# Kernel optimization log

Hardware: AMD Instinct MI355X
Metric: run time of the kernel (lower is better)

## Reference

```python
import jax, jax.numpy as jnp
import numpy as np

B, S, D, E = 2, 2048, 1024, 8
H = 2 * D          # hidden_dim = 2*n_embd
A = H // 16        # adapt_dim


def _ln(x, g, b):
    m = x.mean(-1, keepdims=True)
    v = x.var(-1, keepdims=True)
    return (x - m) * jax.lax.rsqrt(v + 1e-5) * g + b


def setup_inputs() -> dict:
    key = jax.random.key(0)
    ks = jax.random.split(key, 16)
    s = 1.0 / np.sqrt(D)        # shared-linear init scale
    sa = s * 0.01               # adapter-linear init scale
    sg = 0.01 / np.sqrt(A)      # expert adapter init scale
    f32 = jnp.float32
    return {
        "x": jax.random.normal(ks[0], (B, S, D), f32),
        "expert_weights": jax.nn.softmax(jax.random.normal(ks[1], (B * S, E), f32), -1),
        "up_w": jax.random.normal(ks[2], (H, D), f32) * s,
        "gate_w": jax.random.normal(ks[3], (H, D), f32) * s,
        "down_w": jax.random.normal(ks[4], (D, H), f32) * s,
        "pre_w": jax.random.normal(ks[5], (A, D), f32) * sa,
        "post_w": jax.random.normal(ks[6], (A, H), f32) * sa,
        "an_g": jnp.ones((A,), f32),
        "an_b": jnp.zeros((A,), f32),
        "adapt_proj_w": jax.random.normal(ks[7], (H, A), f32) * sa,
        "adapter_w": jax.random.normal(ks[8], (E, A, A), f32) * sg,
        "adapter_g": jnp.ones((E, A), f32),
        "adapter_b": jnp.zeros((E, A), f32),
        "expert_proj_w": jax.random.normal(ks[9], (H, A), f32) * sg,
        "output_proj_w": jax.random.normal(ks[10], (D, H), f32) * sg,
    }


def reference(x, expert_weights, up_w, gate_w, down_w, pre_w, post_w, an_g, an_b,
              adapt_proj_w, adapter_w, adapter_g, adapter_b, expert_proj_w, output_proj_w):
    # ---- SharedExpertMLP ----
    up = x @ up_w.T                                  # [B,S,H]
    gate = x @ gate_w.T                              # [B,S,H]
    hidden = jax.nn.silu(gate) * up                  # SwiGLU
    adapt_in = _ln(x @ pre_w.T, an_g, an_b)          # [B,S,A]
    adapt_out = _ln(hidden @ post_w.T, an_g, an_b)   # [B,S,A]
    w = jnp.einsum('bsa,bta->bst', adapt_in, adapt_out)
    w = jax.nn.silu(jnp.clip(w, -5.0, 5.0))          # clamp+SiLU score
    # explicit fp32 bmm as in original autocast-disabled block
    adapt = jnp.einsum('bst,bta->bsa',
                       w.astype(jnp.float32),
                       adapt_in.astype(jnp.float32)).astype(x.dtype)
    hidden = hidden + 0.1 * (adapt @ adapt_proj_w.T)
    shared_out = hidden @ down_w.T                   # [B,S,D] (dropout is identity in eval)

    # ---- per-token expert mixing ----
    xf = x.reshape(-1, x.shape[-1])                  # [N,D], N=B*S
    a = _ln(xf @ pre_w.T, an_g, an_b)                # [N,A]
    h = jnp.einsum('na,eca->nec', a, adapter_w)      # per-expert low-rank adapt [N,E,A]
    h = _ln(h, adapter_g[None], adapter_b[None])
    mixed = jnp.einsum('ne,nea->na', expert_weights, h)   # combine experts [N,A]
    out = (mixed @ expert_proj_w.T) @ output_proj_w.T     # [N,D]
    return shared_out + out.reshape(x.shape)
```

## Files before the change

### kernel.cpp

```cpp
#include <hip/hip_runtime.h>
#include <hip/hip_bf16.h>
#include <math.h>

#define Bq 2
#define Sq 2048
#define Dq 1024
#define Eq 8
#define Hq 2048
#define Aq 128
#define Nq (Bq*Sq)

typedef __attribute__((ext_vector_type(4))) float f32x4;
typedef __attribute__((ext_vector_type(8))) short bfrag;

__device__ __forceinline__ float silu_f(float x) {
    return x / (1.0f + expf(-x));
}
__device__ __forceinline__ unsigned short f2bf(float x) {
    unsigned u = __float_as_uint(x);
    u += 0x7fffu + ((u >> 16) & 1u);
    return (unsigned short)(u >> 16);
}
__device__ __forceinline__ float bf2f(unsigned short h) {
    return __uint_as_float(((unsigned)h) << 16);
}
__device__ __forceinline__ void gl16(const unsigned short* g, unsigned short* l) {
    __builtin_amdgcn_global_load_lds(
        (const __attribute__((address_space(1))) void*)g,
        (__attribute__((address_space(3))) void*)(void*)l, 16, 0, 0);
}

#define WAITV_BAR(N)                                            \
    asm volatile("s_waitcnt vmcnt(" #N ")" ::: "memory");       \
    __builtin_amdgcn_s_barrier();                               \
    asm volatile("" ::: "memory")
#define END_BAR()                                               \
    asm volatile("" ::: "memory");                              \
    __builtin_amdgcn_s_barrier();                               \
    asm volatile("" ::: "memory")
#define WAITV(N) asm volatile("s_waitcnt vmcnt(" #N ")" ::: "memory")
#define BARF()                                                  \
    asm volatile("" ::: "memory");                              \
    __builtin_amdgcn_s_barrier();                               \
    asm volatile("" ::: "memory")

__global__ __launch_bounds__(256)
void convert_all(const float* __restrict__ x,  const float* __restrict__ gw,
                 const float* __restrict__ uw, const float* __restrict__ dw,
                 const float* __restrict__ pw, const float* __restrict__ ow,
                 const float* __restrict__ opw, const float* __restrict__ aw,
                 const float* __restrict__ apw, const float* __restrict__ epw,
                 unsigned short* xh,  unsigned short* gwh, unsigned short* uwh,
                 unsigned short* dwh, unsigned short* pwh, unsigned short* powh,
                 unsigned short* oph, unsigned short* adw, unsigned short* apT)
{
    __shared__ float t[32][33];
    if (blockIdx.x >= 2048) {
        int bid = blockIdx.x - 2048;
        int z   = bid >> 8;
        int rem = bid & 255;
        int bx  = rem & 3, by = rem >> 2;
        const float* in = z ? epw : apw;
        unsigned short* out = apT + (size_t)z * Hq * Aq;
        int tx = threadIdx.x & 31, ty = threadIdx.x >> 5;
        int r0 = by * 32, c0 = bx * 32;
#pragma unroll
        for (int j = 0; j < 4; j++)
            t[ty + j * 8][tx] = in[(size_t)(r0 + ty + j * 8) * Aq + c0 + tx];
        __syncthreads();
#pragma unroll
        for (int j = 0; j < 4; j++)
            out[(size_t)(c0 + ty + j * 8) * Hq + r0 + tx] = f2bf(t[tx][ty + j * 8]);
        return;
    }
    const int T = 3276800;
    for (int i = blockIdx.x * 256 + threadIdx.x; i < T; i += 2048 * 256) {
        const float* in; unsigned short* hi; int j = i;
        if (j < 1048576)                 { in = x;   hi = xh;  }
        else if ((j -= 1048576) < 524288){ in = gw;  hi = gwh; }
        else if ((j -= 524288) < 524288) { in = uw;  hi = uwh; }
        else if ((j -= 524288) < 524288) { in = dw;  hi = dwh; }
        else if ((j -= 524288) < 32768)  { in = pw;  hi = pwh; }
        else if ((j -= 32768) < 65536)   { in = ow;  hi = powh; }
        else if ((j -= 65536) < 524288)  { in = opw; hi = oph; }
        else { j -= 524288;                in = aw;  hi = adw; }
        float4 v = ((const float4*)in)[j];
        ((ushort4*)hi)[j] = make_ushort4(f2bf(v.x), f2bf(v.y), f2bf(v.z), f2bf(v.w));
    }
}

template<int EPI>
__global__ __launch_bounds__(512)
void mg(const unsigned short* __restrict__ Ah, const unsigned short* __restrict__ Bh,
        void* __restrict__ Cv, int N, int K, int kchunks,
        long zA, long zB, long zC, long pz)
{
    __shared__ __align__(16) unsigned short lds[32768];

    const int tid = threadIdx.x;
    const int l   = tid & 63;
    const int w   = tid >> 6;
    const int wr  = w >> 2, wc = w & 3;
    const int bm0 = blockIdx.y * 128, bn0 = blockIdx.x * 128;
    const int bz  = blockIdx.z / kchunks;
    const int kz  = blockIdx.z - bz * kchunks;
    const int kcnt = K / kchunks;
    const int kbeg = kz * kcnt;
    const int kend = kbeg + kcnt;

    const unsigned short* A0 = Ah + (size_t)bz * zA;
    const unsigned short* B0 = Bh + (size_t)bz * zB;

    const int srow = tid >> 3;
    const int sq   = (tid & 7) ^ (srow & 7);
    const size_t aoff = (size_t)(bm0 + srow) * K + sq * 8;
    const size_t boff = (size_t)(bn0 + srow) * K + sq * 8;
    const size_t r64  = (size_t)64 * K;

    auto stage = [&](int b, int kt) {
        unsigned short* d = &lds[b * 16384 + (w << 9)];
        gl16(A0 + aoff + kt,       d + 0);
        gl16(A0 + aoff + kt + r64, d + 4096);
        gl16(B0 + boff + kt,       d + 8192);
        gl16(B0 + boff + kt + r64, d + 12288);
    };

    const int rowa = (wr * 64 + (l & 15)) * 64;
    const int rowb = (wc * 32 + (l & 15)) * 64;
    const int q0 = (((l >> 4)    ) ^ (l & 7)) << 3;
    const int q1 = (((l >> 4) + 4) ^ (l & 7)) << 3;

    f32x4 acc[4][2];
#pragma unroll
    for (int i = 0; i < 4; i++)
#pragma unroll
        for (int j = 0; j < 2; j++) acc[i][j] = (f32x4){0.f, 0.f, 0.f, 0.f};

    stage(0, kbeg);
    int cur = 0;
    for (int kt = kbeg; kt < kend; kt += 64) {
        if (kt + 64 < kend) {
            stage(cur ^ 1, kt + 64);
            WAITV_BAR(4);
        } else {
            WAITV_BAR(0);
        }
        const int cb = cur * 16384;
#pragma unroll
        for (int ks = 0; ks < 2; ks++) {
            const int qo = ks ? q1 : q0;
            bfrag a4[4], b4[2];
#pragma unroll
            for (int f = 0; f < 4; f++)
                a4[f] = *(const bfrag*)&lds[cb + rowa + f * 1024 + qo];
#pragma unroll
            for (int f = 0; f < 2; f++)
                b4[f] = *(const bfrag*)&lds[cb + 8192 + rowb + f * 1024 + qo];
#pragma unroll
            for (int i = 0; i < 4; i++)
#pragma unroll
                for (int j = 0; j < 2; j++)
                    acc[i][j] = __builtin_amdgcn_mfma_f32_16x16x32_bf16(a4[i], b4[j], acc[i][j], 0, 0, 0);
        }
        END_BAR();
        cur ^= 1;
    }

    const int crow0 = bm0 + wr * 64 + (l >> 4) * 4;
    const int ccol0 = bn0 + wc * 32 + (l & 15);
#pragma unroll
    for (int i = 0; i < 4; i++)
#pragma unroll
        for (int j = 0; j < 2; j++)
#pragma unroll
            for (int r = 0; r < 4; r++) {
                size_t idx = (size_t)(crow0 + i * 16 + r) * N + (ccol0 + j * 16);
                float v = acc[i][j][r];
                if (EPI == 0)
                    ((float*)Cv + (size_t)bz * zC + (size_t)kz * pz)[idx] = v;
                else if (EPI == 1)
                    ((unsigned short*)Cv + (size_t)bz * zC)[idx] =
                        f2bf(silu_f(fminf(fmaxf(v, -5.f), 5.f)));
                else
                    ((unsigned short*)Cv + (size_t)bz * zC)[idx] = f2bf(v);
            }
}

__global__ __launch_bounds__(512)
void gsc(const unsigned short* __restrict__ ainh, const unsigned short* __restrict__ aouth,
         const unsigned short* __restrict__ ainT, float* __restrict__ p3)
{
    __shared__ __align__(16) unsigned short lds[65536];
    const int AIN = 0, AOUT = 16384, AINT = 32768, PB = 49152;

    const int tid = threadIdx.x;
    const int l   = tid & 63;
    const int w   = tid >> 6;
    const int wr  = w >> 2, wc = w & 3;
    const int tz  = blockIdx.x;
    const int ib  = blockIdx.y;
    const int b   = blockIdx.z;
    const long SA = (long)Sq * Aq;

    auto stage32 = [&](int base, const unsigned short* src, size_t kstride) {
#pragma unroll
        for (int rd = 0; rd < 4; rd++) {
            int grow = rd * 32 + (w << 2) + (l >> 4);
            int slot = (l & 15) ^ (grow & 15);
            gl16(src + (size_t)grow * kstride + slot * 8,
                 &lds[base + rd * 4096 + (w << 9)]);
        }
    };

    const unsigned short* ainI_src = ainh + (size_t)b * SA + (size_t)(ib * 128) * Aq;
    f32x4 acc2[4][2];
#pragma unroll
    for (int i = 0; i < 4; i++)
#pragma unroll
        for (int j = 0; j < 2; j++) acc2[i][j] = (f32x4){0.f, 0.f, 0.f, 0.f};

    {
        int tglob = tz * 2;
        stage32(AIN,  ainI_src, Aq);
        stage32(AOUT, aouth + (size_t)b * SA + (size_t)(tglob * 128) * Aq, Aq);
        stage32(AINT, ainT  + (size_t)b * SA + (size_t)(tglob * 128), Sq);
        WAITV_BAR(0);
    }

    const int rowa = (wr * 64 + (l & 15)) * 128;
    const int rowb = (wc * 32 + (l & 15)) * 128;

#pragma unroll 1
    for (int t = 0; t < 2; t++) {
        if (t == 1) {
            int tglob = tz * 2 + 1;
            stage32(AOUT, aouth + (size_t)b * SA + (size_t)(tglob * 128) * Aq, Aq);
            stage32(AINT, ainT  + (size_t)b * SA + (size_t)(tglob * 128), Sq);
            WAITV_BAR(0);
        }
        f32x4 acc1[4][2];
#pragma unroll
        for (int i = 0; i < 4; i++)
#pragma unroll
            for (int j = 0; j < 2; j++) acc1[i][j] = (f32x4){0.f, 0.f, 0.f, 0.f};
#pragma unroll
        for (int ks = 0; ks < 4; ks++) {
            const int qo = ((ks * 4 + (l >> 4)) ^ (l & 15)) << 3;
            bfrag a4[4], b4[2];
#pragma unroll
            for (int f = 0; f < 4; f++)
                a4[f] = *(const bfrag*)&lds[AIN + rowa + f * 2048 + qo];
#pragma unroll
            for (int f = 0; f < 2; f++)
                b4[f] = *(const bfrag*)&lds[AOUT + rowb + f * 2048 + qo];
#pragma unroll
            for (int i = 0; i < 4; i++)
#pragma unroll
                for (int j = 0; j < 2; j++)
                    acc1[i][j] = __builtin_amdgcn_mfma_f32_16x16x32_bf16(a4[i], b4[j], acc1[i][j], 0, 0, 0);
        }
        {
            const int prow0 = wr * 64 + (l >> 4) * 4;
            const int pcol0 = wc * 32 + (l & 15);
#pragma unroll
            for (int i = 0; i < 4; i++)
#pragma unroll
                for (int j = 0; j < 2; j++)
#pragma unroll
                    for (int r = 0; r < 4; r++) {
                        int pr = prow0 + i * 16 + r;
                        int pc = pcol0 + j * 16;
                        float v = silu_f(fminf(fmaxf(acc1[i][j][r], -5.f), 5.f));
                        lds[PB + pr * 128 + (((pc >> 3) ^ (pr & 15)) << 3) + (pc & 7)] = f2bf(v);
                    }
        }
        __syncthreads();
#pragma unroll
        for (int ks = 0; ks < 4; ks++) {
            const int qo = ((ks * 4 + (l >> 4)) ^ (l & 15)) << 3;
            bfrag a4[4], b4[2];
#pragma unroll
            for (int f = 0; f < 4; f++)
                a4[f] = *(const bfrag*)&lds[PB + rowa + f * 2048 + qo];
#pragma unroll
            for (int f = 0; f < 2; f++)
                b4[f] = *(const bfrag*)&lds[AINT + rowb + f * 2048 + qo];
#pragma unroll
            for (int i = 0; i < 4; i++)
#pragma unroll
                for (int j = 0; j < 2; j++)
                    acc2[i][j] = __builtin_amdgcn_mfma_f32_16x16x32_bf16(a4[i], b4[j], acc2[i][j], 0, 0, 0);
        }
        __syncthreads();
    }

    const int crow0 = wr * 64 + (l >> 4) * 4;
    const int ccol0 = wc * 32 + (l & 15);
    float* dst = p3 + ((size_t)(b * 8 + tz) * Sq + ib * 128) * Aq;
#pragma unroll
    for (int i = 0; i < 4; i++)
#pragma unroll
        for (int j = 0; j < 2; j++)
#pragma unroll
            for (int r = 0; r < 4; r++)
                dst[(size_t)(crow0 + i * 16 + r) * Aq + ccol0 + j * 16] = acc2[i][j][r];
}

__global__ __launch_bounds__(512)
void gup(const unsigned short* __restrict__ xh, const unsigned short* __restrict__ gwh,
         const unsigned short* __restrict__ uwh, unsigned short* __restrict__ hh)
{
    __shared__ __align__(16) unsigned short lds[65536];
    const int tid = threadIdx.x;
    const int l   = tid & 63;
    const int w   = tid >> 6;
    const int wr  = w >> 2;
    const int wc  = w & 3;

    int id  = blockIdx.y * gridDim.x + blockIdx.x;
    int xcd = id & 7, j0 = id >> 3;
    int bx  = (xcd & 3) * 4 + (j0 & 3);
    int by  = (xcd >> 2) * 8 + (j0 >> 2);
    const int bm0 = by * 256, bn0 = bx * 128;

    const int srw = tid >> 3;
    const int sq  = (tid & 7) ^ (srw & 7);
    auto stageU = [&](int b, int u, int kt) {
        unsigned short* d = &lds[b * 32768 + u * 8192 + (tid << 3)];
        const unsigned short* src = (u < 2) ? xh : (u == 2 ? gwh : uwh);
        int baserow = (u < 2) ? (bm0 + u * 128) : bn0;
        size_t o = (size_t)(baserow + srw) * Dq + kt + sq * 8;
        gl16(src + o,                   d);
        gl16(src + o + (size_t)64 * Dq, d + 4096);
    };

    const int rowa = (wr * 128 + (l & 15)) * 64;
    const int rowb = (wc * 32  + (l & 15)) * 64;
    const int q0 = (((l >> 4)    ) ^ (l & 7)) << 3;
    const int q1 = (((l >> 4) + 4) ^ (l & 7)) << 3;

    f32x4 accg[8][2], accu[8][2];
#pragma unroll
    for (int i = 0; i < 8; i++)
#pragma unroll
        for (int jj = 0; jj < 2; jj++) {
            accg[i][jj] = (f32x4){0.f, 0.f, 0.f, 0.f};
            accu[i][jj] = (f32x4){0.f, 0.f, 0.f, 0.f};
        }

    stageU(0, 0, 0); stageU(0, 1, 0); stageU(0, 2, 0); stageU(0, 3, 0);
    int cur = 0;
    for (int kt = 0; kt < Dq; kt += 64) {
        const int pf = (kt + 64 < Dq);
        const int cb = cur * 32768;
        const int nx = cur ^ 1;
        bfrag a4[8], b4[2];

        WAITV(2);
        BARF();
#pragma unroll
        for (int f = 0; f < 8; f++)
            a4[f] = *(const bfrag*)&lds[cb + rowa + f * 1024 + q0];
#pragma unroll
        for (int f = 0; f < 2; f++)
            b4[f] = *(const bfrag*)&lds[cb + 16384 + rowb + f * 1024 + q0];
        if (pf) stageU(nx, 0, kt + 64);
        __builtin_amdgcn_s_setprio(1);
#pragma unroll
        for (int i = 0; i < 8; i++)
#pragma unroll
            for (int jj = 0; jj < 2; jj++)
                accg[i][jj] = __builtin_amdgcn_mfma_f32_16x16x32_bf16(a4[i], b4[jj], accg[i][jj], 0, 0, 0);
        __builtin_amdgcn_s_setprio(0);

        if (pf) { WAITV(2); } else { WAITV(0); }
        BARF();
#pragma unroll
        for (int f = 0; f < 2; f++)
            b4[f] = *(const bfrag*)&lds[cb + 24576 + rowb + f * 1024 + q0];
        if (pf) stageU(nx, 1, kt + 64);
        __builtin_amdgcn_s_setprio(1);
#pragma unroll
        for (int i = 0; i < 8; i++)
#pragma unroll
            for (int jj = 0; jj < 2; jj++)
                accu[i][jj] = __builtin_amdgcn_mfma_f32_16x16x32_bf16(a4[i], b4[jj], accu[i][jj], 0, 0, 0);
        __builtin_amdgcn_s_setprio(0);

        BARF();
#pragma unroll
        for (int f = 0; f < 8; f++)
            a4[f] = *(const bfrag*)&lds[cb + rowa + f * 1024 + q1];
#pragma unroll
        for (int f = 0; f < 2; f++)
            b4[f] = *(const bfrag*)&lds[cb + 16384 + rowb + f * 1024 + q1];
        if (pf) stageU(nx, 2, kt + 64);
        __builtin_amdgcn_s_setprio(1);
#pragma unroll
        for (int i = 0; i < 8; i++)
#pragma unroll
            for (int jj = 0; jj < 2; jj++)
                accg[i][jj] = __builtin_amdgcn_mfma_f32_16x16x32_bf16(a4[i], b4[jj], accg[i][jj], 0, 0, 0);
        __builtin_amdgcn_s_setprio(0);

        BARF();
#pragma unroll
        for (int f = 0; f < 2; f++)
            b4[f] = *(const bfrag*)&lds[cb + 24576 + rowb + f * 1024 + q1];
        if (pf) stageU(nx, 3, kt + 64);
        __builtin_amdgcn_s_setprio(1);
#pragma unroll
        for (int i = 0; i < 8; i++)
#pragma unroll
            for (int jj = 0; jj < 2; jj++)
                accu[i][jj] = __builtin_amdgcn_mfma_f32_16x16x32_bf16(a4[i], b4[jj], accu[i][jj], 0, 0, 0);
        __builtin_amdgcn_s_setprio(0);

        cur = nx;
    }

    const int crow0 = bm0 + wr * 128 + (l >> 4) * 4;
    const int ccol0 = bn0 + wc * 32 + (l & 15);
#pragma unroll
    for (int i = 0; i < 8; i++)
#pragma unroll
        for (int jj = 0; jj < 2; jj++)
#pragma unroll
            for (int r = 0; r < 4; r++) {
                size_t idx = (size_t)(crow0 + i * 16 + r) * Hq + (ccol0 + jj * 16);
                hh[idx] = f2bf(silu_f(accg[i][jj][r]) * accu[i][jj][r]);
            }
}

__global__ __launch_bounds__(512)
void gfinal(const unsigned short* __restrict__ hh, const unsigned short* __restrict__ dwh,
            const unsigned short* __restrict__ acat, const unsigned short* __restrict__ kcat,
            float* __restrict__ out)
{
    __shared__ __align__(16) unsigned short lds[49152];
    const int tid = threadIdx.x;
    const int l   = tid & 63;
    const int w   = tid >> 6;
    const int wr  = w >> 2, wc = w & 3;

    int nb  = gridDim.x * gridDim.y;
    int id  = blockIdx.y * gridDim.x + blockIdx.x;
    int id2 = (id & 7) * (nb >> 3) + (id >> 3);
    int bx  = id2 % gridDim.x, by = id2 / gridDim.x;
    const int bm0 = by * 128, bn0 = bx * 128;

    const int srow = tid >> 3;
    const int sq   = (tid & 7) ^ (srow & 7);
    const int rowa = (wr * 64 + (l & 15)) * 64;
    const int rowb = (wc * 32 + (l & 15)) * 64;
    const int q0 = (((l >> 4)    ) ^ (l & 7)) << 3;
    const int q1 = (((l >> 4) + 4) ^ (l & 7)) << 3;

    f32x4 acc[4][2];
#pragma unroll
    for (int i = 0; i < 4; i++)
#pragma unroll
        for (int j = 0; j < 2; j++) acc[i][j] = (f32x4){0.f, 0.f, 0.f, 0.f};

    {
        const size_t aoff = (size_t)(bm0 + srow) * Hq + sq * 8;
        const size_t boff = (size_t)(bn0 + srow) * Hq + sq * 8;
        const size_t r64  = (size_t)64 * Hq;
        auto stage = [&](int b, int kt) {
            unsigned short* d = &lds[b * 16384 + (w << 9)];
            gl16(hh  + aoff + kt,       d + 0);
            gl16(hh  + aoff + kt + r64, d + 4096);
            gl16(dwh + boff + kt,       d + 8192);
            gl16(dwh + boff + kt + r64, d + 12288);
        };
        stage(0, 0);
        stage(1, 64);
        int cur = 0;
        for (int kt = 0; kt < Hq; kt += 64) {
            if (kt + 64 < Hq) { WAITV_BAR(4); } else { WAITV_BAR(0); }
            if (kt + 128 < Hq) {
                int nb3 = (cur + 2 >= 3) ? cur - 1 : cur + 2;
                stage(nb3, kt + 128);
            }
            const int cb = cur * 16384;
#pragma unroll
            for (int ks = 0; ks < 2; ks++) {
                const int qo = ks ? q1 : q0;
                bfrag a4[4], b4[2];
#pragma unroll
                for (int f = 0; f < 4; f++)
                    a4[f] = *(const bfrag*)&lds[cb + rowa + f * 1024 + qo];
#pragma unroll
                for (int f = 0; f < 2; f++)
                    b4[f] = *(const bfrag*)&lds[cb + 8192 + rowb + f * 1024 + qo];
#pragma unroll
                for (int i = 0; i < 4; i++)
#pragma unroll
                    for (int j = 0; j < 2; j++)
                        acc[i][j] = __builtin_amdgcn_mfma_f32_16x16x32_bf16(a4[i], b4[j], acc[i][j], 0, 0, 0);
            }
            cur = (cur == 2) ? 0 : cur + 1;
        }
    }
    END_BAR();
    {
        const size_t aoff = (size_t)(bm0 + srow) * 256 + sq * 8;
        const size_t boff = (size_t)(bn0 + srow) * 256 + sq * 8;
        const size_t r64  = (size_t)64 * 256;
        auto stage2 = [&](int b, int kt) {
            unsigned short* d = &lds[b * 16384 + (w << 9)];
            gl16(acat + aoff + kt,       d + 0);
            gl16(acat + aoff + kt + r64, d + 4096);
            gl16(kcat + boff + kt,       d + 8192);
            gl16(kcat + boff + kt + r64, d + 12288);
        };
        stage2(0, 0);
        stage2(1, 64);
        int cur = 0;
        for (int kt = 0; kt < 256; kt += 64) {
            if (kt + 64 < 256) { WAITV_BAR(4); } else { WAITV_BAR(0); }
            if (kt + 128 < 256) {
                int nb3 = (cur + 2 >= 3) ? cur - 1 : cur + 2;
                stage2(nb3, kt + 128);
            }
            const int cb = cur * 16384;
#pragma unroll
            for (int ks = 0; ks < 2; ks++) {
                const int qo = ks ? q1 : q0;
                bfrag a4[4], b4[2];
#pragma unroll
                for (int f = 0; f < 4; f++)
                    a4[f] = *(const bfrag*)&lds[cb + rowa + f * 1024 + qo];
#pragma unroll
                for (int f = 0; f < 2; f++)
                    b4[f] = *(const bfrag*)&lds[cb + 8192 + rowb + f * 1024 + qo];
#pragma unroll
                for (int i = 0; i < 4; i++)
#pragma unroll
                    for (int j = 0; j < 2; j++)
                        acc[i][j] = __builtin_amdgcn_mfma_f32_16x16x32_bf16(a4[i], b4[j], acc[i][j], 0, 0, 0);
            }
            cur = (cur == 2) ? 0 : cur + 1;
        }
    }

    const int crow0 = bm0 + wr * 64 + (l >> 4) * 4;
    const int ccol0 = bn0 + wc * 32 + (l & 15);
#pragma unroll
    for (int i = 0; i < 4; i++)
#pragma unroll
        for (int j = 0; j < 2; j++)
#pragma unroll
            for (int r = 0; r < 4; r++)
                out[(size_t)(crow0 + i * 16 + r) * Dq + ccol0 + j * 16] = acc[i][j][r];
}

template<int NZ, bool WT>
__global__ __launch_bounds__(256)
void rln(const float* __restrict__ p, unsigned short* __restrict__ oh,
         unsigned short* __restrict__ aT,
         const float* __restrict__ g, const float* __restrict__ b, long pstride)
{
    int row  = blockIdx.x * 4 + (threadIdx.x >> 6);
    int lane = threadIdx.x & 63;
    long base = (long)row * Aq;
    float x0 = 0.f, x1 = 0.f;
#pragma unroll
    for (int z = 0; z < NZ; z++) {
        x0 += p[base + z * pstride + lane];
        x1 += p[base + z * pstride + lane + 64];
    }
    float s  = x0 + x1;
    float ss = x0 * x0 + x1 * x1;
#pragma unroll
    for (int off = 32; off > 0; off >>= 1) {
        s  += __shfl_xor(s, off);
        ss += __shfl_xor(ss, off);
    }
    float m  = s * (1.0f / Aq);
    float v  = ss * (1.0f / Aq) - m * m;
    float rs = rsqrtf(v + 1e-5f);
    unsigned short h0 = f2bf((x0 - m) * rs * g[lane]      + b[lane]);
    unsigned short h1 = f2bf((x1 - m) * rs * g[lane + 64] + b[lane + 64]);
    oh[base + lane]      = h0;
    oh[base + lane + 64] = h1;
    if (WT) {
        int bb2 = row >> 11, sidx = row & 2047;
        unsigned short* t = aT + (size_t)bb2 * Sq * Aq + sidx;
        t[(size_t)lane * Sq]        = h0;
        t[(size_t)(lane + 64) * Sq] = h1;
    }
}

template<int NZ>
__global__ __launch_bounds__(256)
void rbf(const float* __restrict__ p, unsigned short* __restrict__ o,
         int rowsPerB, float scale, int total, int ostride, int ocol, int ocolStep)
{
    int i = blockIdx.x * 256 + threadIdx.x;
    if (i >= total) return;
    int n = i >> 7, a = i & 127;
    int bz = n / rowsPerB, s = n - bz * rowsPerB;
    long base = ((long)bz * NZ) * rowsPerB * Aq + (long)s * Aq + a;
    float acc = 0.f;
#pragma unroll
    for (int z = 0; z < NZ; z++) acc += p[base + (long)z * rowsPerB * Aq];
    o[(long)s * ostride + (ocol + bz * ocolStep) + a +
      (ocolStep ? 0 : (long)bz * rowsPerB * ostride)] = f2bf(acc * scale);
}

__global__ __launch_bounds__(256)
void tailk(const float* __restrict__ p3, const unsigned short* __restrict__ he,
           const float* __restrict__ ew, const float* __restrict__ g,
           const float* __restrict__ bb, unsigned short* __restrict__ acat)
{
    if (blockIdx.x < 2048) {
        int i = blockIdx.x * 256 + threadIdx.x;
        int n = i >> 7, a = i & 127;
        int bz = n >> 11, s = n & 2047;
        long base = ((long)bz * 8) * Sq * Aq + (long)s * Aq + a;
        float acc = 0.f;
#pragma unroll
        for (int z = 0; z < 8; z++) acc += p3[base + (long)z * Sq * Aq];
        acat[(long)n * 256 + a] = f2bf(acc * 0.1f);
        return;
    }
    int n    = (blockIdx.x - 2048) * 4 + (threadIdx.x >> 6);
    int lane = threadIdx.x & 63;
    float a0 = 0.0f, a1 = 0.0f;
#pragma unroll
    for (int e = 0; e < Eq; e++) {
        const unsigned short* r = he + ((long)e * Nq + n) * Aq;
        float x0 = bf2f(r[lane]), x1 = bf2f(r[lane + 64]);
        float s  = x0 + x1;
        float ss = x0 * x0 + x1 * x1;
#pragma unroll
        for (int off = 32; off > 0; off >>= 1) {
            s  += __shfl_xor(s, off);
            ss += __shfl_xor(ss, off);
        }
        float m  = s * (1.0f / Aq);
        float v  = ss * (1.0f / Aq) - m * m;
        float rs = rsqrtf(v + 1e-5f);
        float wv = ew[(long)n * Eq + e];
        a0 += wv * ((x0 - m) * rs * g[e * Aq + lane]      + bb[e * Aq + lane]);
        a1 += wv * ((x1 - m) * rs * g[e * Aq + lane + 64] + bb[e * Aq + lane + 64]);
    }
    acat[(long)n * 256 + 128 + lane]      = f2bf(a0);
    acat[(long)n * 256 + 128 + lane + 64] = f2bf(a1);
}

extern "C" void kernel_launch(void* const* d_in, const int* in_sizes, int n_in,
                              void* d_out, int out_size, void* d_ws, size_t ws_size,
                              hipStream_t stream)
{
    const float* x             = (const float*)d_in[0];
    const float* ew            = (const float*)d_in[1];
    const float* up_w          = (const float*)d_in[2];
    const float* gate_w        = (const float*)d_in[3];
    const float* down_w        = (const float*)d_in[4];
    const float* pre_w         = (const float*)d_in[5];
    const float* post_w        = (const float*)d_in[6];
    const float* an_g          = (const float*)d_in[7];
    const float* an_b          = (const float*)d_in[8];
    const float* adapt_proj_w  = (const float*)d_in[9];
    const float* adapter_w     = (const float*)d_in[10];
    const float* adapter_g     = (const float*)d_in[11];
    const float* adapter_b     = (const float*)d_in[12];
    const float* expert_proj_w = (const float*)d_in[13];
    const float* output_proj_w = (const float*)d_in[14];
    float* out = (float*)d_out;

#define OFF(kb) ((char*)d_ws + (size_t)(kb) * 1024)
    float* kdp  = (float*)OFF(0);
    float* p1   = (float*)OFF(16384);
    float* p2   = (float*)OFF(0);
    float* p3   = (float*)OFF(0);
    unsigned short* he = (unsigned short*)OFF(16384);
    unsigned short* hh   = (unsigned short*)OFF(32768);
    unsigned short* xh   = (unsigned short*)OFF(49152);
    unsigned short* gwh  = (unsigned short*)OFF(57344);
    unsigned short* uwh  = (unsigned short*)OFF(61440);
    unsigned short* dwh  = (unsigned short*)OFF(65536);
    unsigned short* oph  = (unsigned short*)OFF(69632);
    unsigned short* pwh  = (unsigned short*)OFF(73728);
    unsigned short* powh = (unsigned short*)OFF(73984);
    unsigned short* apT  = (unsigned short*)OFF(74496);
    unsigned short* epT  = (unsigned short*)OFF(75008);
    unsigned short* ainh = (unsigned short*)OFF(75520);
    unsigned short* ainT = (unsigned short*)OFF(76544);
    unsigned short* aouth= (unsigned short*)OFF(77568);
    unsigned short* adw  = (unsigned short*)OFF(78592);
    unsigned short* kcat = (unsigned short*)OFF(78848);
    unsigned short* acat = (unsigned short*)OFF(79360);
#undef OFF
    (void)epT;

    dim3 blk(256), blk512(512);
    const long NA = (long)Nq * Aq;

    convert_all<<<dim3(2560), blk, 0, stream>>>(x, gate_w, up_w, down_w, pre_w,
        post_w, output_proj_w, adapter_w, adapt_proj_w, expert_proj_w,
        xh, gwh, uwh, dwh, pwh, powh, oph, adw, apT);

    mg<0><<<dim3(1, 8, 32), blk512, 0, stream>>>(dwh, apT, kdp, Aq, Hq, 16,
        (long)Dq * Hq, (long)Aq * Hq, (long)16 * Dq * Aq, (long)Dq * Aq);
    rbf<16><<<dim3(1024), blk, 0, stream>>>(kdp, kcat, Dq, 1.0f, 2 * Dq * Aq, 256, 0, 128);

    mg<0><<<dim3(1, 32, 8), blk512, 0, stream>>>(xh, pwh, p1, Aq, Dq, 8, 0, 0, 0, NA);
    rln<8, true><<<dim3(1024), blk, 0, stream>>>(p1, ainh, ainT, an_g, an_b, NA);

    mg<2><<<dim3(1, 32, 8), blk512, 0, stream>>>(ainh, adw, he, Aq, Aq, 1,
        0, (long)Aq * Aq, NA, 0);

    gup<<<dim3(16, 16), blk512, 0, stream>>>(xh, gwh, uwh, hh);

    mg<0><<<dim3(1, 32, 8), blk512, 0, stream>>>(hh, powh, p2, Aq, Hq, 8, 0, 0, 0, NA);
    rln<8, false><<<dim3(1024), blk, 0, stream>>>(p2, aouth, nullptr, an_g, an_b, NA);

    gsc<<<dim3(8, 16, 2), blk512, 0, stream>>>(ainh, aouth, ainT, p3);

    tailk<<<dim3(3072), blk, 0, stream>>>(p3, he, ew, adapter_g, adapter_b, acat);

    gfinal<<<dim3(8, 32), blk512, 0, stream>>>(hh, dwh, acat, kcat, out);
}
```

Before: 159.8 us.

## Merge independent GEMM and reduce launches; interleave prefetch with MFMA in final GEMM

Two independent split-K GEMMs (down-proj times adapt-proj and x times pre_w) are merged into one launch with block-index dispatch. Their two reduction/LayerNorm follow-ups are also merged into one kernel. This removes two kernel launches and the idle tail between them. The final GEMM main loop now splits each k-tile into two half-steps, issues the A and B prefetches separately between MFMA batches, and raises wave priority around the MFMAs to overlap loads with compute. The cost is an extra barrier per half-step.

```diff
diff --git a/kernel.cpp b/kernel.cpp
--- a/kernel.cpp
+++ b/kernel.cpp
@@ -187,6 +187,111 @@
 }
 
 __global__ __launch_bounds__(512)
+void mgpair(const unsigned short* __restrict__ dwh, const unsigned short* __restrict__ apT,
+            float* __restrict__ kdp,
+            const unsigned short* __restrict__ xh, const unsigned short* __restrict__ pwh,
+            float* __restrict__ p1)
+{
+    __shared__ __align__(16) unsigned short lds[32768];
+
+    const int tid = threadIdx.x;
+    const int l   = tid & 63;
+    const int w   = tid >> 6;
+    const int wr  = w >> 2, wc = w & 3;
+
+    const unsigned short *Ah, *Bh; float* Cv;
+    int K, kchunks, by, zidx;
+    long zA, zB, zC, pz;
+    int bid = blockIdx.x;
+    if (bid < 256) {
+        Ah = dwh; Bh = apT; Cv = kdp; K = Hq; kchunks = 16;
+        zA = (long)Dq * Hq; zB = (long)Aq * Hq; zC = (long)16 * Dq * Aq; pz = (long)Dq * Aq;
+        by = bid & 7; zidx = bid >> 3;
+    } else {
+        int r = bid - 256;
+        Ah = xh; Bh = pwh; Cv = p1; K = Dq; kchunks = 8;
+        zA = 0; zB = 0; zC = 0; pz = (long)Nq * Aq;
+        by = r & 31; zidx = r >> 5;
+    }
+    const int N = Aq;
+    const int bm0 = by * 128, bn0 = 0;
+    const int bz  = zidx / kchunks;
+    const int kz  = zidx - bz * kchunks;
+    const int kcnt = K / kchunks;
+    const int kbeg = kz * kcnt;
+    const int kend = kbeg + kcnt;
+
+    const unsigned short* A0 = Ah + (size_t)bz * zA;
+    const unsigned short* B0 = Bh + (size_t)bz * zB;
+
+    const int srow = tid >> 3;
+    const int sq   = (tid & 7) ^ (srow & 7);
+    const size_t aoff = (size_t)(bm0 + srow) * K + sq * 8;
+    const size_t boff = (size_t)(bn0 + srow) * K + sq * 8;
+    const size_t r64  = (size_t)64 * K;
+
+    auto stage = [&](int b, int kt) {
+        unsigned short* d = &lds[b * 16384 + (w << 9)];
+        gl16(A0 + aoff + kt,       d + 0);
+        gl16(A0 + aoff + kt + r64, d + 4096);
+        gl16(B0 + boff + kt,       d + 8192);
+        gl16(B0 + boff + kt + r64, d + 12288);
+    };
+
+    const int rowa = (wr * 64 + (l & 15)) * 64;
+    const int rowb = (wc * 32 + (l & 15)) * 64;
+    const int q0 = (((l >> 4)    ) ^ (l & 7)) << 3;
+    const int q1 = (((l >> 4) + 4) ^ (l & 7)) << 3;
+
+    f32x4 acc[4][2];
+#pragma unroll
+    for (int i = 0; i < 4; i++)
+#pragma unroll
+        for (int j = 0; j < 2; j++) acc[i][j] = (f32x4){0.f, 0.f, 0.f, 0.f};
+
+    stage(0, kbeg);
+    int cur = 0;
+    for (int kt = kbeg; kt < kend; kt += 64) {
+        if (kt + 64 < kend) {
+            stage(cur ^ 1, kt + 64);
+            WAITV_BAR(4);
+        } else {
+            WAITV_BAR(0);
+        }
+        const int cb = cur * 16384;
+#pragma unroll
+        for (int ks = 0; ks < 2; ks++) {
+            const int qo = ks ? q1 : q0;
+            bfrag a4[4], b4[2];
+#pragma unroll
+            for (int f = 0; f < 4; f++)
+                a4[f] = *(const bfrag*)&lds[cb + rowa + f * 1024 + qo];
+#pragma unroll
+            for (int f = 0; f < 2; f++)
+                b4[f] = *(const bfrag*)&lds[cb + 8192 + rowb + f * 1024 + qo];
+#pragma unroll
+            for (int i = 0; i < 4; i++)
+#pragma unroll
+                for (int j = 0; j < 2; j++)
+                    acc[i][j] = __builtin_amdgcn_mfma_f32_16x16x32_bf16(a4[i], b4[j], acc[i][j], 0, 0, 0);
+        }
+        END_BAR();
+        cur ^= 1;
+    }
+
+    const int crow0 = bm0 + wr * 64 + (l >> 4) * 4;
+    const int ccol0 = bn0 + wc * 32 + (l & 15);
+    float* C = Cv + (size_t)bz * zC + (size_t)kz * pz;
+#pragma unroll
+    for (int i = 0; i < 4; i++)
+#pragma unroll
+        for (int j = 0; j < 2; j++)
+#pragma unroll
+            for (int r = 0; r < 4; r++)
+                C[(size_t)(crow0 + i * 16 + r) * N + (ccol0 + j * 16)] = acc[i][j][r];
+}
+
+__global__ __launch_bounds__(512)
 void gsc(const unsigned short* __restrict__ ainh, const unsigned short* __restrict__ aouth,
          const unsigned short* __restrict__ ainT, float* __restrict__ p3)
 {
@@ -466,39 +571,54 @@
         const size_t aoff = (size_t)(bm0 + srow) * Hq + sq * 8;
         const size_t boff = (size_t)(bn0 + srow) * Hq + sq * 8;
         const size_t r64  = (size_t)64 * Hq;
-        auto stage = [&](int b, int kt) {
+        auto stageA = [&](int b, int kt) {
             unsigned short* d = &lds[b * 16384 + (w << 9)];
-            gl16(hh  + aoff + kt,       d + 0);
-            gl16(hh  + aoff + kt + r64, d + 4096);
+            gl16(hh + aoff + kt,       d + 0);
+            gl16(hh + aoff + kt + r64, d + 4096);
+        };
+        auto stageB = [&](int b, int kt) {
+            unsigned short* d = &lds[b * 16384 + (w << 9)];
             gl16(dwh + boff + kt,       d + 8192);
             gl16(dwh + boff + kt + r64, d + 12288);
         };
-        stage(0, 0);
-        stage(1, 64);
+        stageA(0, 0);  stageB(0, 0);
+        stageA(1, 64); stageB(1, 64);
         int cur = 0;
         for (int kt = 0; kt < Hq; kt += 64) {
             if (kt + 64 < Hq) { WAITV_BAR(4); } else { WAITV_BAR(0); }
-            if (kt + 128 < Hq) {
-                int nb3 = (cur + 2 >= 3) ? cur - 1 : cur + 2;
-                stage(nb3, kt + 128);
-            }
-            const int cb = cur * 16384;
-#pragma unroll
-            for (int ks = 0; ks < 2; ks++) {
-                const int qo = ks ? q1 : q0;
-                bfrag a4[4], b4[2];
-#pragma unroll
-                for (int f = 0; f < 4; f++)
-                    a4[f] = *(const bfrag*)&lds[cb + rowa + f * 1024 + qo];
-#pragma unroll
-                for (int f = 0; f < 2; f++)
-                    b4[f] = *(const bfrag*)&lds[cb + 8192 + rowb + f * 1024 + qo];
-#pragma unroll
-                for (int i = 0; i < 4; i++)
-#pragma unroll
-                    for (int j = 0; j < 2; j++)
-                        acc[i][j] = __builtin_amdgcn_mfma_f32_16x16x32_bf16(a4[i], b4[j], acc[i][j], 0, 0, 0);
-            }
+            const int pf  = (kt + 128 < Hq);
+            const int nb3 = (cur + 2 >= 3) ? cur - 1 : cur + 2;
+            const int cb  = cur * 16384;
+            bfrag a4[4], b4[2];
+#pragma unroll
+            for (int f = 0; f < 4; f++)
+                a4[f] = *(const bfrag*)&lds[cb + rowa + f * 1024 + q0];
+#pragma unroll
+            for (int f = 0; f < 2; f++)
+                b4[f] = *(const bfrag*)&lds[cb + 8192 + rowb + f * 1024 + q0];
+            if (pf) stageA(nb3, kt + 128);
+            __builtin_amdgcn_s_setprio(1);
+#pragma unroll
+            for (int i = 0; i < 4; i++)
+#pragma unroll
+                for (int j = 0; j < 2; j++)
+                    acc[i][j] = __builtin_amdgcn_mfma_f32_16x16x32_bf16(a4[i], b4[j], acc[i][j], 0, 0, 0);
+            __builtin_amdgcn_s_setprio(0);
+            BARF();
+#pragma unroll
+            for (int f = 0; f < 4; f++)
+                a4[f] = *(const bfrag*)&lds[cb + rowa + f * 1024 + q1];
+#pragma unroll
+            for (int f = 0; f < 2; f++)
+                b4[f] = *(const bfrag*)&lds[cb + 8192 + rowb + f * 1024 + q1];
+            if (pf) stageB(nb3, kt + 128);
+            __builtin_amdgcn_s_setprio(1);
+#pragma unroll
+            for (int i = 0; i < 4; i++)
+#pragma unroll
+                for (int j = 0; j < 2; j++)
+                    acc[i][j] = __builtin_amdgcn_mfma_f32_16x16x32_bf16(a4[i], b4[j], acc[i][j], 0, 0, 0);
+            __builtin_amdgcn_s_setprio(0);
             cur = (cur == 2) ? 0 : cur + 1;
         }
     }
@@ -592,21 +712,50 @@
     }
 }
 
-template<int NZ>
 __global__ __launch_bounds__(256)
-void rbf(const float* __restrict__ p, unsigned short* __restrict__ o,
-         int rowsPerB, float scale, int total, int ostride, int ocol, int ocolStep)
-{
-    int i = blockIdx.x * 256 + threadIdx.x;
-    if (i >= total) return;
-    int n = i >> 7, a = i & 127;
-    int bz = n / rowsPerB, s = n - bz * rowsPerB;
-    long base = ((long)bz * NZ) * rowsPerB * Aq + (long)s * Aq + a;
-    float acc = 0.f;
-#pragma unroll
-    for (int z = 0; z < NZ; z++) acc += p[base + (long)z * rowsPerB * Aq];
-    o[(long)s * ostride + (ocol + bz * ocolStep) + a +
-      (ocolStep ? 0 : (long)bz * rowsPerB * ostride)] = f2bf(acc * scale);
+void rlnrbf(const float* __restrict__ kdp, const float* __restrict__ p1,
+            unsigned short* __restrict__ kcat,
+            unsigned short* __restrict__ ainh, unsigned short* __restrict__ ainT,
+            const float* __restrict__ g, const float* __restrict__ b)
+{
+    if (blockIdx.x < 1024) {
+        int i = blockIdx.x * 256 + threadIdx.x;
+        int n = i >> 7, a = i & 127;
+        int bz = n >> 10, s = n & 1023;
+        long base = (long)bz * 16 * Dq * Aq + (long)s * Aq + a;
+        float acc = 0.f;
+#pragma unroll
+        for (int z = 0; z < 16; z++) acc += kdp[base + (long)z * Dq * Aq];
+        kcat[(long)s * 256 + bz * 128 + a] = f2bf(acc);
+        return;
+    }
+    int row  = (blockIdx.x - 1024) * 4 + (threadIdx.x >> 6);
+    int lane = threadIdx.x & 63;
+    long base = (long)row * Aq;
+    float x0 = 0.f, x1 = 0.f;
+#pragma unroll
+    for (int z = 0; z < 8; z++) {
+        x0 += p1[base + (long)z * Nq * Aq + lane];
+        x1 += p1[base + (long)z * Nq * Aq + lane + 64];
+    }
+    float s  = x0 + x1;
+    float ss = x0 * x0 + x1 * x1;
+#pragma unroll
+    for (int off = 32; off > 0; off >>= 1) {
+        s  += __shfl_xor(s, off);
+        ss += __shfl_xor(ss, off);
+    }
+    float m  = s * (1.0f / Aq);
+    float v  = ss * (1.0f / Aq) - m * m;
+    float rs = rsqrtf(v + 1e-5f);
+    unsigned short h0 = f2bf((x0 - m) * rs * g[lane]      + b[lane]);
+    unsigned short h1 = f2bf((x1 - m) * rs * g[lane + 64] + b[lane + 64]);
+    ainh[base + lane]      = h0;
+    ainh[base + lane + 64] = h1;
+    int bb2 = row >> 11, sidx = row & 2047;
+    unsigned short* t = ainT + (size_t)bb2 * Sq * Aq + sidx;
+    t[(size_t)lane * Sq]        = h0;
+    t[(size_t)(lane + 64) * Sq] = h1;
 }
 
 __global__ __launch_bounds__(256)
@@ -703,12 +852,9 @@
         post_w, output_proj_w, adapter_w, adapt_proj_w, expert_proj_w,
         xh, gwh, uwh, dwh, pwh, powh, oph, adw, apT);
 
-    mg<0><<<dim3(1, 8, 32), blk512, 0, stream>>>(dwh, apT, kdp, Aq, Hq, 16,
-        (long)Dq * Hq, (long)Aq * Hq, (long)16 * Dq * Aq, (long)Dq * Aq);
-    rbf<16><<<dim3(1024), blk, 0, stream>>>(kdp, kcat, Dq, 1.0f, 2 * Dq * Aq, 256, 0, 128);
-
-    mg<0><<<dim3(1, 32, 8), blk512, 0, stream>>>(xh, pwh, p1, Aq, Dq, 8, 0, 0, 0, NA);
-    rln<8, true><<<dim3(1024), blk, 0, stream>>>(p1, ainh, ainT, an_g, an_b, NA);
+    mgpair<<<dim3(512), blk512, 0, stream>>>(dwh, apT, kdp, xh, pwh, p1);
+
+    rlnrbf<<<dim3(2048), blk, 0, stream>>>(kdp, p1, kcat, ainh, ainT, an_g, an_b);
 
     mg<2><<<dim3(1, 32, 8), blk512, 0, stream>>>(ainh, adw, he, Aq, Aq, 1,
         0, (long)Aq * Aq, NA, 0);
```

Result: faster. 154.0 us (-3.6%).
